# Performance work log

Hardware: AMD Instinct MI355X
Metric: run time of the kernel (lower is better)

## Reference

```python
import jax, jax.numpy as jnp
import numpy as np

# ---- module config (matches __init__ defaults) ----
NUM_EL_FULL = 128
LV_START, LV_END = 31, 95
NUM_S = LV_END - LV_START            # 64 sensors
NX = NY = 408
ROI = 128
DX = DY = 0.0002
C0 = 1500.0
FS = 40.0e6
DT = 1.0 / FS
R_IN = 0.0406
ARC_ANGLE = 270.0
ARC_START = 135.0
T_SAMPLES = 2030
BATCH = 64


def _geometry():
    """Reproduce _precompute_geometry + _precompute_time_indices_and_weights in numpy."""
    spacing = ARC_ANGLE / (NUM_EL_FULL - 1)
    all_ang = ARC_START + np.arange(NUM_EL_FULL) * spacing
    ang = all_ang[LV_START:LV_END]
    ang_rad = ang * np.pi / 180.0
    cx = (NX / 2 - 0.5) * DX
    cy = (NY / 2 - 0.5) * DY
    sx = cx + R_IN * np.cos(ang_rad)
    sy = cy + R_IN * np.sin(ang_rad)

    rsx = round((NX - ROI) / 2)
    rsy = round((NY - ROI) / 2)
    x_pos = (np.arange(rsx, rsx + ROI, dtype=np.float32) * DX)
    y_pos = (np.arange(rsy, rsy + ROI, dtype=np.float32) * DY)
    yg, xg = np.meshgrid(y_pos, x_pos, indexing='ij')  # [ROI, ROI]

    x_diff = xg[..., None] - sx[None, None, :]          # [ROI, ROI, S]
    y_diff = yg[..., None] - sy[None, None, :]
    dist = np.sqrt(x_diff ** 2 + y_diff ** 2)
    t_idx = np.round(dist / C0 / DT).astype(np.int32)

    normal = ang_rad + np.pi
    a2p = np.arctan2(y_diff, x_diff)
    adiff = a2p - normal[None, None, :]
    adiff = np.arctan2(np.sin(adiff), np.cos(adiff))
    weights = np.clip(np.cos(adiff), 0.0, None).astype(np.float32)
    valid = (t_idx >= 0) & (t_idx < T_SAMPLES)
    return t_idx, weights, valid


def setup_inputs() -> dict:
    key = jax.random.key(0)
    t_idx, weights, valid = _geometry()
    sinogram = jax.random.normal(key, (BATCH, 1, NUM_S, T_SAMPLES), dtype=jnp.float32)
    return {
        "sinogram": sinogram,
        "weights": jnp.asarray(weights),
        "time_indices": jnp.asarray(t_idx),
        "valid_mask": jnp.asarray(valid),
    }


def reference(sinogram, weights, time_indices, valid_mask):
    """DAS beamforming, output_type='both', norm_type='clamp'."""
    B = sinogram.shape[0]
    T = sinogram.shape[-1]
    sino = sinogram[:, 0]                                   # [B, S, T]
    S = sino.shape[1]
    t = jnp.clip(time_indices, 0, T - 1)                    # [H, W, S]
    sensor_idx = jnp.arange(S)[None, None, :]               # [1, 1, S]
    # gather: per-pixel, per-sensor time sample -> [B, H, W, S]
    sampled = sino[:, sensor_idx, t]
    w = jnp.where(valid_mask, weights, 0.0)                 # mask * weight fused
    weighted = sampled * w[None]                            # [B, H, W, S]

    das = weighted.sum(axis=3)[:, None]                     # [B, 1, H, W]
    # normalize: clamp to >=0, per-batch max
    das = jnp.maximum(das, 0.0)
    m = das.reshape(B, -1).max(axis=1)
    m = jnp.where(m > 1e-8, m, 1.0)
    das = das / m[:, None, None, None]

    pixel_interp = jnp.transpose(weighted, (0, 3, 1, 2))    # [B, S, H, W]
    return das, pixel_interp
```

## Files before the change

### kernel.cpp

```cpp
#include <hip/hip_runtime.h>
#include <stdint.h>

#define NB   64
#define NS   64
#define NT   2030
#define NP   16384
#define DAS_ELEMS (NB * NP)
#define PIX_ELEMS ((size_t)NB * NS * NP)

typedef float v4f __attribute__((ext_vector_type(4)));

__global__ __launch_bounds__(256) void prep_kernel(
    const int* __restrict__ t_idx, const float* __restrict__ w,
    int* __restrict__ tc, float* __restrict__ wv)
{
    __shared__ int   ti[64][65];
    __shared__ float wf[64][65];
    const int pbase = blockIdx.x * 64;

    #pragma unroll
    for (int k = 0; k < 16; ++k) {
        int o = k * 256 + threadIdx.x;
        int r = o >> 6, s = o & 63;
        ti[r][s] = t_idx[pbase * 64 + o];
        wf[r][s] = w[pbase * 64 + o];
    }
    __syncthreads();

    #pragma unroll
    for (int k = 0; k < 16; ++k) {
        int o = k * 256 + threadIdx.x;
        int s = o >> 6, r = o & 63;
        int t = ti[r][s];
        bool valid = (t >= 0) & (t < NT);
        int tcl = min(max(t, 0), NT - 1);
        tc[s * NP + pbase + r] = tcl;
        wv[s * NP + pbase + r] = valid ? wf[r][s] : 0.0f;
    }
}

template <bool TR>
__global__ __launch_bounds__(256) void main_kernel(
    const float* __restrict__ sino,
    const int*   __restrict__ tptr,
    const float* __restrict__ wptr,
    float*       __restrict__ das,
    float*       __restrict__ pix,
    unsigned*    __restrict__ bmax)
{
    const int b = blockIdx.y;
    const int p = blockIdx.x * 1024 + threadIdx.x * 4;
    const float* __restrict__ srow = sino + (size_t)b * (NS * NT);
    float* __restrict__ pixb = pix + (size_t)b * ((size_t)NS * NP) + p;

    v4f acc = (v4f)(0.0f);

    for (int s = 0; s < NS; ++s) {
        int4 t; float wx, wy, wz, ww;
        if (TR) {
            t = *(const int4*)(tptr + s * NP + p);
            const float4 w4 = *(const float4*)(wptr + s * NP + p);
            wx = w4.x; wy = w4.y; wz = w4.z; ww = w4.w;
        } else {
            int t0 = tptr[(p + 0) * NS + s];
            int t1 = tptr[(p + 1) * NS + s];
            int t2 = tptr[(p + 2) * NS + s];
            int t3 = tptr[(p + 3) * NS + s];
            wx = ((t0 >= 0) & (t0 < NT)) ? wptr[(p + 0) * NS + s] : 0.f;
            wy = ((t1 >= 0) & (t1 < NT)) ? wptr[(p + 1) * NS + s] : 0.f;
            wz = ((t2 >= 0) & (t2 < NT)) ? wptr[(p + 2) * NS + s] : 0.f;
            ww = ((t3 >= 0) & (t3 < NT)) ? wptr[(p + 3) * NS + s] : 0.f;
            t.x = min(max(t0, 0), NT - 1);
            t.y = min(max(t1, 0), NT - 1);
            t.z = min(max(t2, 0), NT - 1);
            t.w = min(max(t3, 0), NT - 1);
        }
        const float* __restrict__ sr = srow + s * NT;
        v4f v;
        v.x = sr[t.x] * wx;
        v.y = sr[t.y] * wy;
        v.z = sr[t.z] * wz;
        v.w = sr[t.w] * ww;
        __builtin_nontemporal_store(v, (v4f*)(pixb + (size_t)s * NP));
        acc += v;
    }

    acc.x = fmaxf(acc.x, 0.f); acc.y = fmaxf(acc.y, 0.f);
    acc.z = fmaxf(acc.z, 0.f); acc.w = fmaxf(acc.w, 0.f);
    *(v4f*)(das + (size_t)b * NP + p) = acc;

    float m = fmaxf(fmaxf(acc.x, acc.y), fmaxf(acc.z, acc.w));
    #pragma unroll
    for (int off = 32; off > 0; off >>= 1)
        m = fmaxf(m, __shfl_down(m, off, 64));
    __shared__ float wm[4];
    if ((threadIdx.x & 63) == 0) wm[threadIdx.x >> 6] = m;
    __syncthreads();
    if (threadIdx.x == 0) {
        m = fmaxf(fmaxf(wm[0], wm[1]), fmaxf(wm[2], wm[3]));
        atomicMax(&bmax[b], __float_as_uint(m));
    }
}

__global__ __launch_bounds__(256) void norm_kernel(
    float* __restrict__ das, const unsigned* __restrict__ bmax)
{
    int idx = (blockIdx.x * 256 + threadIdx.x) * 4;
    int b = idx >> 14;
    float m = __uint_as_float(bmax[b]);
    m = (m > 1e-8f) ? m : 1.0f;
    v4f v = *(v4f*)(das + idx);
    v.x = v.x / m; v.y = v.y / m; v.z = v.z / m; v.w = v.w / m;
    *(v4f*)(das + idx) = v;
}

extern "C" void kernel_launch(void* const* d_in, const int* in_sizes, int n_in,
                              void* d_out, int out_size, void* d_ws, size_t ws_size,
                              hipStream_t stream)
{
    const float* sino  = (const float*)d_in[0];
    const float* w     = (const float*)d_in[1];
    const int*   t_idx = (const int*)  d_in[2];

    float* das = (float*)d_out;
    float* pix = (float*)d_out + DAS_ELEMS;

    char* ws = (char*)d_ws;
    const size_t need = (size_t)(8u << 20) + 256;
    const bool big = ws_size >= need;

    unsigned* bmax;
    int* tc = nullptr; float* wv = nullptr;
    if (big) {
        tc   = (int*)ws;
        wv   = (float*)(ws + (4u << 20));
        bmax = (unsigned*)(ws + (8u << 20));
    } else {
        bmax = (unsigned*)ws;
    }

    (void)hipMemsetAsync(bmax, 0, NB * sizeof(unsigned), stream);

    if (big) {
        prep_kernel<<<256, 256, 0, stream>>>(t_idx, w, tc, wv);
        main_kernel<true><<<dim3(16, NB), 256, 0, stream>>>(sino, tc, wv, das, pix, bmax);
    } else {
        main_kernel<false><<<dim3(16, NB), 256, 0, stream>>>(sino, t_idx, w, das, pix, bmax);
    }
    norm_kernel<<<DAS_ELEMS / 1024, 256, 0, stream>>>(das, bmax);
}
```

Baseline: 373.0 us.

## Stage sinogram rows in double-buffered LDS and process 2048 pixels per block

The main kernel now copies each sensor's sinogram row (2030 floats) into shared memory with double buffering and does the per-pixel time gather from LDS instead of global memory. Each block covers 2048 pixels (8 pixels per thread), so grid.x drops from 16 to 8 and each staged row is reused across more pixels. This replaces scattered global/L2 gathers with LDS reads and adds a __syncthreads per sensor iteration. The kernel is dominated by the 268 MB pixel_interp output write, so the gain may be small. The non-transposed fallback path is left functionally unchanged.

```diff
diff --git a/kernel.cpp b/kernel.cpp
--- a/kernel.cpp
+++ b/kernel.cpp
@@ -6,7 +6,6 @@
 #define NT   2030
 #define NP   16384
 #define DAS_ELEMS (NB * NP)
-#define PIX_ELEMS ((size_t)NB * NS * NP)
 
 typedef float v4f __attribute__((ext_vector_type(4)));
 
@@ -39,8 +38,80 @@
     }
 }
 
-template <bool TR>
-__global__ __launch_bounds__(256) void main_kernel(
+static __device__ __forceinline__ void stage_row(
+    float* __restrict__ dst, const float* __restrict__ src, int tid)
+{
+    const float2* __restrict__ s2 = (const float2*)src;
+    float2* __restrict__ d2 = (float2*)dst;
+    #pragma unroll
+    for (int k = 0; k < 4; ++k) {
+        int idx = tid + k * 256;
+        if (idx < 1015) d2[idx] = s2[idx];
+    }
+}
+
+__global__ __launch_bounds__(256) void main2_kernel(
+    const float* __restrict__ sino,
+    const int*   __restrict__ tc,
+    const float* __restrict__ wv,
+    float*       __restrict__ das,
+    float*       __restrict__ pix,
+    unsigned*    __restrict__ bmax)
+{
+    __shared__ __align__(16) float row[2][2048];
+    const int b   = blockIdx.y;
+    const int tid = threadIdx.x;
+    const int p   = blockIdx.x * 2048 + tid * 4;
+    const float* __restrict__ srow = sino + (size_t)b * (NS * NT);
+    float* __restrict__ pixb = pix + (size_t)b * ((size_t)NS * NP);
+
+    stage_row(row[0], srow, tid);
+
+    v4f acc0 = (v4f)(0.0f), acc1 = (v4f)(0.0f);
+
+    for (int s = 0; s < NS; ++s) {
+        __syncthreads();
+        if (s + 1 < NS) stage_row(row[(s + 1) & 1], srow + (s + 1) * NT, tid);
+
+        const float* __restrict__ r = row[s & 1];
+        const int4   ta = *(const int4*)  (tc + s * NP + p);
+        const float4 wa = *(const float4*)(wv + s * NP + p);
+        const int4   tb = *(const int4*)  (tc + s * NP + p + 1024);
+        const float4 wb = *(const float4*)(wv + s * NP + p + 1024);
+
+        v4f va, vb;
+        va.x = r[ta.x] * wa.x; va.y = r[ta.y] * wa.y;
+        va.z = r[ta.z] * wa.z; va.w = r[ta.w] * wa.w;
+        vb.x = r[tb.x] * wb.x; vb.y = r[tb.y] * wb.y;
+        vb.z = r[tb.z] * wb.z; vb.w = r[tb.w] * wb.w;
+
+        __builtin_nontemporal_store(va, (v4f*)(pixb + (size_t)s * NP + p));
+        __builtin_nontemporal_store(vb, (v4f*)(pixb + (size_t)s * NP + p + 1024));
+        acc0 += va; acc1 += vb;
+    }
+
+    acc0.x = fmaxf(acc0.x, 0.f); acc0.y = fmaxf(acc0.y, 0.f);
+    acc0.z = fmaxf(acc0.z, 0.f); acc0.w = fmaxf(acc0.w, 0.f);
+    acc1.x = fmaxf(acc1.x, 0.f); acc1.y = fmaxf(acc1.y, 0.f);
+    acc1.z = fmaxf(acc1.z, 0.f); acc1.w = fmaxf(acc1.w, 0.f);
+    *(v4f*)(das + (size_t)b * NP + p)        = acc0;
+    *(v4f*)(das + (size_t)b * NP + p + 1024) = acc1;
+
+    float m = fmaxf(fmaxf(fmaxf(acc0.x, acc0.y), fmaxf(acc0.z, acc0.w)),
+                    fmaxf(fmaxf(acc1.x, acc1.y), fmaxf(acc1.z, acc1.w)));
+    #pragma unroll
+    for (int off = 32; off > 0; off >>= 1)
+        m = fmaxf(m, __shfl_down(m, off, 64));
+    __shared__ float wm[4];
+    if ((tid & 63) == 0) wm[tid >> 6] = m;
+    __syncthreads();
+    if (tid == 0) {
+        m = fmaxf(fmaxf(wm[0], wm[1]), fmaxf(wm[2], wm[3]));
+        atomicMax(&bmax[b], __float_as_uint(m));
+    }
+}
+
+__global__ __launch_bounds__(256) void main_fallback_kernel(
     const float* __restrict__ sino,
     const int*   __restrict__ tptr,
     const float* __restrict__ wptr,
@@ -54,37 +125,24 @@
     float* __restrict__ pixb = pix + (size_t)b * ((size_t)NS * NP) + p;
 
     v4f acc = (v4f)(0.0f);
-
     for (int s = 0; s < NS; ++s) {
-        int4 t; float wx, wy, wz, ww;
-        if (TR) {
-            t = *(const int4*)(tptr + s * NP + p);
-            const float4 w4 = *(const float4*)(wptr + s * NP + p);
-            wx = w4.x; wy = w4.y; wz = w4.z; ww = w4.w;
-        } else {
-            int t0 = tptr[(p + 0) * NS + s];
-            int t1 = tptr[(p + 1) * NS + s];
-            int t2 = tptr[(p + 2) * NS + s];
-            int t3 = tptr[(p + 3) * NS + s];
-            wx = ((t0 >= 0) & (t0 < NT)) ? wptr[(p + 0) * NS + s] : 0.f;
-            wy = ((t1 >= 0) & (t1 < NT)) ? wptr[(p + 1) * NS + s] : 0.f;
-            wz = ((t2 >= 0) & (t2 < NT)) ? wptr[(p + 2) * NS + s] : 0.f;
-            ww = ((t3 >= 0) & (t3 < NT)) ? wptr[(p + 3) * NS + s] : 0.f;
-            t.x = min(max(t0, 0), NT - 1);
-            t.y = min(max(t1, 0), NT - 1);
-            t.z = min(max(t2, 0), NT - 1);
-            t.w = min(max(t3, 0), NT - 1);
-        }
+        int t0 = tptr[(p + 0) * NS + s];
+        int t1 = tptr[(p + 1) * NS + s];
+        int t2 = tptr[(p + 2) * NS + s];
+        int t3 = tptr[(p + 3) * NS + s];
+        float wx = ((t0 >= 0) & (t0 < NT)) ? wptr[(p + 0) * NS + s] : 0.f;
+        float wy = ((t1 >= 0) & (t1 < NT)) ? wptr[(p + 1) * NS + s] : 0.f;
+        float wz = ((t2 >= 0) & (t2 < NT)) ? wptr[(p + 2) * NS + s] : 0.f;
+        float ww = ((t3 >= 0) & (t3 < NT)) ? wptr[(p + 3) * NS + s] : 0.f;
         const float* __restrict__ sr = srow + s * NT;
         v4f v;
-        v.x = sr[t.x] * wx;
-        v.y = sr[t.y] * wy;
-        v.z = sr[t.z] * wz;
-        v.w = sr[t.w] * ww;
+        v.x = sr[min(max(t0, 0), NT - 1)] * wx;
+        v.y = sr[min(max(t1, 0), NT - 1)] * wy;
+        v.z = sr[min(max(t2, 0), NT - 1)] * wz;
+        v.w = sr[min(max(t3, 0), NT - 1)] * ww;
         __builtin_nontemporal_store(v, (v4f*)(pixb + (size_t)s * NP));
         acc += v;
     }
-
     acc.x = fmaxf(acc.x, 0.f); acc.y = fmaxf(acc.y, 0.f);
     acc.z = fmaxf(acc.z, 0.f); acc.w = fmaxf(acc.w, 0.f);
     *(v4f*)(das + (size_t)b * NP + p) = acc;
@@ -143,9 +201,9 @@
 
     if (big) {
         prep_kernel<<<256, 256, 0, stream>>>(t_idx, w, tc, wv);
-        main_kernel<true><<<dim3(16, NB), 256, 0, stream>>>(sino, tc, wv, das, pix, bmax);
+        main2_kernel<<<dim3(8, NB), 256, 0, stream>>>(sino, tc, wv, das, pix, bmax);
     } else {
-        main_kernel<false><<<dim3(16, NB), 256, 0, stream>>>(sino, t_idx, w, das, pix, bmax);
+        main_fallback_kernel<<<dim3(16, NB), 256, 0, stream>>>(sino, t_idx, w, das, pix, bmax);
     }
     norm_kernel<<<DAS_ELEMS / 1024, 256, 0, stream>>>(das, bmax);
 }
```

New measurement: 448.4 us. 20.2% more time.
